# Optimization experiments

Measured on AMD Instinct MI355X. Metric: run time of the kernel, lower is better.

The kernel has to match this reference:

```python
import jax, jax.numpy as jnp
import numpy as np

N = 50000      # nodes
E = 800000     # edges (before self loops)
F_IN = 128
HID = 32
HEADS = 4
OUT_DIM = 1
NEG_SLOPE = 0.2


def gat_conv(x, edge_src, edge_dst, W, a_src, a_dst, bias):
    """PyG GATConv (concat=True, self-loops already appended to edge lists).
    x: [N, Fin], W: [Fin, H*D], a_src/a_dst: [H, D], bias: [H*D]."""
    H, D = a_src.shape
    h = (x @ W).reshape(N, H, D)                      # [N, H, D]
    alpha_src = jnp.einsum('nhd,hd->nh', h, a_src)    # [N, H]
    alpha_dst = jnp.einsum('nhd,hd->nh', h, a_dst)    # [N, H]
    e = alpha_src[edge_src] + alpha_dst[edge_dst]     # [Et, H]
    e = jnp.where(e > 0, e, NEG_SLOPE * e)            # leaky_relu(0.2)
    # softmax over edges grouped by destination node
    m = jax.ops.segment_max(e, edge_dst, num_segments=N)  # [N, H]
    e = jnp.exp(e - jax.lax.stop_gradient(m)[edge_dst])
    s = jax.ops.segment_sum(e, edge_dst, num_segments=N)  # [N, H]
    alpha = e / (s[edge_dst] + 1e-16)                 # [Et, H]
    msg = h[edge_src] * alpha[:, :, None]             # [Et, H, D]
    out = jax.ops.segment_sum(msg, edge_dst, num_segments=N)  # [N, H, D]
    return out.reshape(N, H * D) + bias


def setup_inputs() -> dict:
    key = jax.random.key(0)
    ks = jax.random.split(key, 16)
    HD = HEADS * HID
    def glorot(k, shape, fan_in):
        return jax.random.normal(k, shape, dtype=jnp.float32) / np.sqrt(fan_in)
    inp = {
        'x': jax.random.normal(ks[0], (N, F_IN), dtype=jnp.float32),
        'edge_index': jax.random.randint(ks[1], (2, E), 0, N, dtype=jnp.int64 if jax.config.jax_enable_x64 else jnp.int32),
        'W1': glorot(ks[2], (F_IN, HD), F_IN),
        'a_src1': glorot(ks[3], (HEADS, HID), HID),
        'a_dst1': glorot(ks[4], (HEADS, HID), HID),
        'b1': jnp.zeros((HD,), dtype=jnp.float32),
        'W2': glorot(ks[5], (HD, HD), HD),
        'a_src2': glorot(ks[6], (HEADS, HID), HID),
        'a_dst2': glorot(ks[7], (HEADS, HID), HID),
        'b2': jnp.zeros((HD,), dtype=jnp.float32),
        'Wc1': glorot(ks[8], (HD, HID), HD),
        'bc1': jnp.zeros((HID,), dtype=jnp.float32),
        'Wc2': glorot(ks[9], (HID, OUT_DIM), HID),
        'bc2': jnp.zeros((OUT_DIM,), dtype=jnp.float32),
    }
    return inp


def reference(x, edge_index, W1, a_src1, a_dst1, b1, W2, a_src2, a_dst2, b2,
              Wc1, bc1, Wc2, bc2):
    # PyG add_self_loops=True: append (i -> i) for every node
    loops = jnp.arange(N, dtype=edge_index.dtype)
    src = jnp.concatenate([edge_index[0], loops])
    dst = jnp.concatenate([edge_index[1], loops])
    h = gat_conv(x, src, dst, W1, a_src1, a_dst1, b1)
    h = jax.nn.relu(h)
    h = gat_conv(h, src, dst, W2, a_src2, a_dst2, b2)
    h = jax.nn.relu(h)
    # classifier (dropout is identity at eval)
    h = h @ Wc1 + bc1
    h = h @ Wc2 + bc2
    return jax.nn.sigmoid(h)
```

## Files before the change

kernel.cpp:

```cpp
#include <hip/hip_runtime.h>
#include <hip/hip_bf16.h>
#include <math.h>

#define NEG_SLOPE 0.2f

__device__ __forceinline__ unsigned short f2bf(float f) {
    unsigned int u = __float_as_uint(f);
    u = (u + 0x7fffu + ((u >> 16) & 1u)) >> 16;
    return (unsigned short)u;
}
__device__ __forceinline__ float bflo(unsigned int p) {
    return __uint_as_float(p << 16);
}
__device__ __forceinline__ float bfhi(unsigned int p) {
    return __uint_as_float(p & 0xffff0000u);
}

__device__ __forceinline__ void gemm_alpha_body(
    float* __restrict__ xt,
    const float* __restrict__ X, const float* __restrict__ W,
    const float* __restrict__ a_src, const float* __restrict__ a_dst,
    unsigned short* __restrict__ Hb, float* __restrict__ as_out,
    float* __restrict__ ad_out, int N, int n0, int t)
{
    {
        const float4* src = (const float4*)(X + (size_t)n0 * 128);
        float4* dst = (float4*)xt;
        int rows = N - n0; if (rows > 32) rows = 32;
        int maxv = rows * 32;
        #pragma unroll
        for (int i = 0; i < 4; ++i) {
            int idx = t + i * 256;
            int g = idx < maxv ? idx : maxv - 1;
            dst[idx] = src[g];
        }
    }
    __syncthreads();

    int rg = t >> 5;
    int c  = t & 31;
    int j0 = c * 4;

    float a00=0.f,a01=0.f,a02=0.f,a03=0.f;
    float a10=0.f,a11=0.f,a12=0.f,a13=0.f;
    float a20=0.f,a21=0.f,a22=0.f,a23=0.f;
    float a30=0.f,a31=0.f,a32=0.f,a33=0.f;

    #pragma unroll 4
    for (int k = 0; k < 128; ++k) {
        float4 w = *(const float4*)(W + k * 128 + j0);
        float x0 = xt[(rg     ) * 128 + k];
        float x1 = xt[(rg +  8) * 128 + k];
        float x2 = xt[(rg + 16) * 128 + k];
        float x3 = xt[(rg + 24) * 128 + k];
        a00 = fmaf(x0, w.x, a00); a01 = fmaf(x0, w.y, a01);
        a02 = fmaf(x0, w.z, a02); a03 = fmaf(x0, w.w, a03);
        a10 = fmaf(x1, w.x, a10); a11 = fmaf(x1, w.y, a11);
        a12 = fmaf(x1, w.z, a12); a13 = fmaf(x1, w.w, a13);
        a20 = fmaf(x2, w.x, a20); a21 = fmaf(x2, w.y, a21);
        a22 = fmaf(x2, w.z, a22); a23 = fmaf(x2, w.w, a23);
        a30 = fmaf(x3, w.x, a30); a31 = fmaf(x3, w.y, a31);
        a32 = fmaf(x3, w.z, a32); a33 = fmaf(x3, w.w, a33);
    }

    float4 asv = *(const float4*)(a_src + j0);
    float4 adv = *(const float4*)(a_dst + j0);
    int head = c >> 3;
    int wlane = (c & 7) == 0;

    #pragma unroll
    for (int rr = 0; rr < 4; ++rr) {
        float b0, b1, b2, b3;
        if (rr == 0) { b0=a00; b1=a01; b2=a02; b3=a03; }
        else if (rr == 1) { b0=a10; b1=a11; b2=a12; b3=a13; }
        else if (rr == 2) { b0=a20; b1=a21; b2=a22; b3=a23; }
        else { b0=a30; b1=a31; b2=a32; b3=a33; }
        int row = n0 + rg + rr * 8;
        bool valid = row < N;
        if (valid) {
            unsigned int lo = (unsigned int)f2bf(b0) | ((unsigned int)f2bf(b1) << 16);
            unsigned int hi = (unsigned int)f2bf(b2) | ((unsigned int)f2bf(b3) << 16);
            *(uint2*)(Hb + (size_t)row * 128 + j0) = make_uint2(lo, hi);
        }
        float ps = b0*asv.x + b1*asv.y + b2*asv.z + b3*asv.w;
        float pd = b0*adv.x + b1*adv.y + b2*adv.z + b3*adv.w;
        ps += __shfl_xor(ps, 1, 64); pd += __shfl_xor(pd, 1, 64);
        ps += __shfl_xor(ps, 2, 64); pd += __shfl_xor(pd, 2, 64);
        ps += __shfl_xor(ps, 4, 64); pd += __shfl_xor(pd, 4, 64);
        if (wlane && valid) {
            as_out[row * 4 + head] = ps;
            ad_out[row * 4 + head] = pd;
        }
    }
}

__global__ __launch_bounds__(256) void gemm_alpha_kernel(
    const float* __restrict__ X, const float* __restrict__ W,
    const float* __restrict__ a_src, const float* __restrict__ a_dst,
    unsigned short* __restrict__ Hb, float* __restrict__ as_out,
    float* __restrict__ ad_out, int N)
{
    __shared__ float xt[32 * 128];
    gemm_alpha_body(xt, X, W, a_src, a_dst, Hb, as_out, ad_out, N,
                    blockIdx.x * 32, threadIdx.x);
}

__global__ __launch_bounds__(256) void gemm_fill_kernel(
    const float* __restrict__ X, const float* __restrict__ W,
    const float* __restrict__ a_src, const float* __restrict__ a_dst,
    unsigned short* __restrict__ Hb, float* __restrict__ as_out,
    float* __restrict__ ad_out, int N,
    const int* __restrict__ esrc, int E, int Et,
    const int* __restrict__ offs, const int* __restrict__ pos,
    int* __restrict__ csr, int gemmBlocks, int NS)
{
    __shared__ float xt[32 * 128];
    int g  = blockIdx.x >> 3;
    int l8 = blockIdx.x & 7;
    if ((g & 1) == 0) {
        int gb = (g >> 1) * 8 + l8;
        if (gb < gemmBlocks)
            gemm_alpha_body(xt, X, W, a_src, a_dst, Hb, as_out, ad_out, N,
                            gb * 32, threadIdx.x);
    } else {
        int slice = g >> 1;
        if (slice >= NS) return;
        int rlo = (int)(((long long)N * l8) >> 3);
        int rhi = (int)(((long long)N * (l8 + 1)) >> 3);
        int csrLo = offs[rlo];
        int csrHi = (rhi < N) ? offs[rhi] : Et;
        int e0 = (int)((long long)Et * slice / NS);
        int e1 = (int)((long long)Et * (slice + 1) / NS);
        for (int e = e0 + threadIdx.x; e < e1; e += 256) {
            int p = pos[e];
            if (p >= csrLo && p < csrHi) {
                int s = (e < E) ? esrc[e] : (e - E);
                csr[p] = s;
            }
        }
    }
}

__global__ __launch_bounds__(256) void zero_int_kernel(int* __restrict__ p, int n)
{
    int i = blockIdx.x * 256 + threadIdx.x;
    if (i < n) p[i] = 0;
}

__global__ __launch_bounds__(256) void count_rank_kernel(
    const int* __restrict__ edst, int E, int Et,
    int* __restrict__ cnt, int* __restrict__ rank)
{
    int e = blockIdx.x * 256 + threadIdx.x;
    if (e >= Et) return;
    int d = (e < E) ? edst[e] : (e - E);
    rank[e] = atomicAdd(&cnt[d], 1);
}

__global__ __launch_bounds__(256) void pos_kernel(
    const int* __restrict__ edst, int E, int Et,
    const int* __restrict__ offs, int* __restrict__ rank)
{
    int e = blockIdx.x * 256 + threadIdx.x;
    if (e >= Et) return;
    int d = (e < E) ? edst[e] : (e - E);
    rank[e] = offs[d] + rank[e];
}

__global__ __launch_bounds__(256) void scan_block_kernel(
    const int* __restrict__ in, int* __restrict__ out,
    int* __restrict__ bsum, int n)
{
    __shared__ int sh[256];
    int i = blockIdx.x * 256 + threadIdx.x;
    int v = (i < n) ? in[i] : 0;
    sh[threadIdx.x] = v;
    __syncthreads();
    #pragma unroll
    for (int off = 1; off < 256; off <<= 1) {
        int t = 0;
        if (threadIdx.x >= off) t = sh[threadIdx.x - off];
        __syncthreads();
        if (threadIdx.x >= off) sh[threadIdx.x] += t;
        __syncthreads();
    }
    if (i < n) out[i] = sh[threadIdx.x] - v;
    if (threadIdx.x == 255) bsum[blockIdx.x] = sh[255];
}

__global__ __launch_bounds__(256) void scan_add_kernel(
    int* __restrict__ offs, const int* __restrict__ bsum, int n)
{
    int i = blockIdx.x * 256 + threadIdx.x;
    if (i < n) offs[i] += bsum[blockIdx.x];
}

__global__ __launch_bounds__(256) void gat_fused_kernel(
    const unsigned short* __restrict__ Hb, const int* __restrict__ csr,
    const int* __restrict__ offs, const int* __restrict__ cnt,
    const float* __restrict__ as, const float* __restrict__ ad,
    const float* __restrict__ bias, float* __restrict__ out, int N)
{
    __shared__ float wtab[4 * 256];
    __shared__ int   stab[4 * 64];

    int t = threadIdx.x;
    int wv = t >> 6;
    int g  = (t >> 4) & 3;
    int q  = t & 15;
    int d = blockIdx.x * 16 + (t >> 4);
    if (d >= N) return;
    int start = offs[d];
    int deg = cnt[d];
    float4 adv = *(const float4*)(ad + d * 4);
    int h = q >> 2;
    int f0 = q * 8;

    float m0 = -INFINITY, m1 = -INFINITY, m2 = -INFINITY, m3 = -INFINITY;
    float s0 = 0.f, s1 = 0.f, s2 = 0.f, s3 = 0.f;
    float acc0=0.f,acc1=0.f,acc2=0.f,acc3=0.f,acc4=0.f,acc5=0.f,acc6=0.f,acc7=0.f;

    const float* wbase = wtab + wv * 256 + g * 4 + h;
    const int*   sbase = stab + wv * 64 + g * 16;

    for (int c0 = 0; c0 < deg; c0 += 16) {
        int rem = deg - c0;
        int len = rem < 16 ? rem : 16;
        bool valid = q < len;
        int sidx = valid ? csr[start + c0 + q] : 0;
        float4 av = *(const float4*)(as + sidx * 4);
        float e0 = av.x + adv.x; e0 = e0 > 0.f ? e0 : NEG_SLOPE * e0;
        float e1 = av.y + adv.y; e1 = e1 > 0.f ? e1 : NEG_SLOPE * e1;
        float e2 = av.z + adv.z; e2 = e2 > 0.f ? e2 : NEG_SLOPE * e2;
        float e3 = av.w + adv.w; e3 = e3 > 0.f ? e3 : NEG_SLOPE * e3;
        if (!valid) { e0 = e1 = e2 = e3 = -INFINITY; }

        float c0m = e0, c1m = e1, c2m = e2, c3m = e3;
        #pragma unroll
        for (int off = 8; off; off >>= 1) {
            c0m = fmaxf(c0m, __shfl_xor(c0m, off, 64));
            c1m = fmaxf(c1m, __shfl_xor(c1m, off, 64));
            c2m = fmaxf(c2m, __shfl_xor(c2m, off, 64));
            c3m = fmaxf(c3m, __shfl_xor(c3m, off, 64));
        }
        float nm0 = fmaxf(m0, c0m), nm1 = fmaxf(m1, c1m);
        float nm2 = fmaxf(m2, c2m), nm3 = fmaxf(m3, c3m);
        float r0 = __expf(m0 - nm0), r1 = __expf(m1 - nm1);
        float r2 = __expf(m2 - nm2), r3 = __expf(m3 - nm3);
        m0 = nm0; m1 = nm1; m2 = nm2; m3 = nm3;

        float w0 = valid ? __expf(e0 - m0) : 0.f;
        float w1 = valid ? __expf(e1 - m1) : 0.f;
        float w2 = valid ? __expf(e2 - m2) : 0.f;
        float w3 = valid ? __expf(e3 - m3) : 0.f;

        float t0 = w0, t1 = w1, t2 = w2, t3 = w3;
        #pragma unroll
        for (int off = 8; off; off >>= 1) {
            t0 += __shfl_xor(t0, off, 64);
            t1 += __shfl_xor(t1, off, 64);
            t2 += __shfl_xor(t2, off, 64);
            t3 += __shfl_xor(t3, off, 64);
        }
        s0 = s0 * r0 + t0; s1 = s1 * r1 + t1;
        s2 = s2 * r2 + t2; s3 = s3 * r3 + t3;
        float rs = h == 0 ? r0 : (h == 1 ? r1 : (h == 2 ? r2 : r3));
        acc0 *= rs; acc1 *= rs; acc2 *= rs; acc3 *= rs;
        acc4 *= rs; acc5 *= rs; acc6 *= rs; acc7 *= rs;

        ((float4*)wtab)[wv * 64 + q * 4 + g] = make_float4(w0, w1, w2, w3);
        stab[wv * 64 + g * 16 + q] = sidx;

        int kk = 0;
        for (; kk + 4 <= len; kk += 4) {
            int sk0 = sbase[kk+0], sk1 = sbase[kk+1];
            int sk2 = sbase[kk+2], sk3 = sbase[kk+3];
            float wa = wbase[(kk+0)*16], wb = wbase[(kk+1)*16];
            float wc = wbase[(kk+2)*16], wd = wbase[(kk+3)*16];
            uint4 p0 = *(const uint4*)(Hb + (size_t)sk0 * 128 + f0);
            uint4 p1 = *(const uint4*)(Hb + (size_t)sk1 * 128 + f0);
            uint4 p2 = *(const uint4*)(Hb + (size_t)sk2 * 128 + f0);
            uint4 p3 = *(const uint4*)(Hb + (size_t)sk3 * 128 + f0);
            acc0 = fmaf(wa, bflo(p0.x), acc0); acc1 = fmaf(wa, bfhi(p0.x), acc1);
            acc2 = fmaf(wa, bflo(p0.y), acc2); acc3 = fmaf(wa, bfhi(p0.y), acc3);
            acc4 = fmaf(wa, bflo(p0.z), acc4); acc5 = fmaf(wa, bfhi(p0.z), acc5);
            acc6 = fmaf(wa, bflo(p0.w), acc6); acc7 = fmaf(wa, bfhi(p0.w), acc7);
            acc0 = fmaf(wb, bflo(p1.x), acc0); acc1 = fmaf(wb, bfhi(p1.x), acc1);
            acc2 = fmaf(wb, bflo(p1.y), acc2); acc3 = fmaf(wb, bfhi(p1.y), acc3);
            acc4 = fmaf(wb, bflo(p1.z), acc4); acc5 = fmaf(wb, bfhi(p1.z), acc5);
            acc6 = fmaf(wb, bflo(p1.w), acc6); acc7 = fmaf(wb, bfhi(p1.w), acc7);
            acc0 = fmaf(wc, bflo(p2.x), acc0); acc1 = fmaf(wc, bfhi(p2.x), acc1);
            acc2 = fmaf(wc, bflo(p2.y), acc2); acc3 = fmaf(wc, bfhi(p2.y), acc3);
            acc4 = fmaf(wc, bflo(p2.z), acc4); acc5 = fmaf(wc, bfhi(p2.z), acc5);
            acc6 = fmaf(wc, bflo(p2.w), acc6); acc7 = fmaf(wc, bfhi(p2.w), acc7);
            acc0 = fmaf(wd, bflo(p3.x), acc0); acc1 = fmaf(wd, bfhi(p3.x), acc1);
            acc2 = fmaf(wd, bflo(p3.y), acc2); acc3 = fmaf(wd, bfhi(p3.y), acc3);
            acc4 = fmaf(wd, bflo(p3.z), acc4); acc5 = fmaf(wd, bfhi(p3.z), acc5);
            acc6 = fmaf(wd, bflo(p3.w), acc6); acc7 = fmaf(wd, bfhi(p3.w), acc7);
        }
        for (; kk < len; ++kk) {
            int sk = sbase[kk];
            float wk = wbase[kk*16];
            uint4 p = *(const uint4*)(Hb + (size_t)sk * 128 + f0);
            acc0 = fmaf(wk, bflo(p.x), acc0); acc1 = fmaf(wk, bfhi(p.x), acc1);
            acc2 = fmaf(wk, bflo(p.y), acc2); acc3 = fmaf(wk, bfhi(p.y), acc3);
            acc4 = fmaf(wk, bflo(p.z), acc4); acc5 = fmaf(wk, bfhi(p.z), acc5);
            acc6 = fmaf(wk, bflo(p.w), acc6); acc7 = fmaf(wk, bfhi(p.w), acc7);
        }
    }

    float sh = h == 0 ? s0 : (h == 1 ? s1 : (h == 2 ? s2 : s3));
    float inv = 1.f / (sh + 1e-16f);
    float4 bA = *(const float4*)(bias + f0);
    float4 bB = *(const float4*)(bias + f0 + 4);
    float4 oA = make_float4(fmaxf(acc0 * inv + bA.x, 0.f),
                            fmaxf(acc1 * inv + bA.y, 0.f),
                            fmaxf(acc2 * inv + bA.z, 0.f),
                            fmaxf(acc3 * inv + bA.w, 0.f));
    float4 oB = make_float4(fmaxf(acc4 * inv + bB.x, 0.f),
                            fmaxf(acc5 * inv + bB.y, 0.f),
                            fmaxf(acc6 * inv + bB.z, 0.f),
                            fmaxf(acc7 * inv + bB.w, 0.f));
    *(float4*)(out + (size_t)d * 128 + f0)     = oA;
    *(float4*)(out + (size_t)d * 128 + f0 + 4) = oB;
}

__global__ __launch_bounds__(256) void classifier_kernel(
    const float* __restrict__ X, const float* __restrict__ Wc1,
    const float* __restrict__ bc1, const float* __restrict__ Wc2,
    const float* __restrict__ bc2, float* __restrict__ out, int N)
{
    int n = blockIdx.x * 8 + (threadIdx.x >> 5);
    if (n >= N) return;
    int j = threadIdx.x & 31;
    const float* xrow = X + (size_t)n * 128;
    float acc = bc1[j];
    #pragma unroll 8
    for (int k = 0; k < 128; ++k)
        acc = fmaf(xrow[k], Wc1[k * 32 + j], acc);
    float y = acc * Wc2[j];
    #pragma unroll
    for (int off = 16; off; off >>= 1) y += __shfl_xor(y, off, 64);
    if (j == 0)
        out[n] = 1.0f / (1.0f + expf(-(y + bc2[0])));
}

extern "C" void kernel_launch(void* const* d_in, const int* in_sizes, int n_in,
                              void* d_out, int out_size, void* d_ws, size_t ws_size,
                              hipStream_t stream)
{
    const float* x      = (const float*)d_in[0];
    const int*   eidx   = (const int*)d_in[1];
    const float* W1     = (const float*)d_in[2];
    const float* a_src1 = (const float*)d_in[3];
    const float* a_dst1 = (const float*)d_in[4];
    const float* b1     = (const float*)d_in[5];
    const float* W2     = (const float*)d_in[6];
    const float* a_src2 = (const float*)d_in[7];
    const float* a_dst2 = (const float*)d_in[8];
    const float* b2     = (const float*)d_in[9];
    const float* Wc1    = (const float*)d_in[10];
    const float* bc1    = (const float*)d_in[11];
    const float* Wc2    = (const float*)d_in[12];
    const float* bc2    = (const float*)d_in[13];

    int N  = in_sizes[0] / 128;
    int E  = in_sizes[1] / 2;
    int Et = E + N;
    const int* esrc = eidx;
    const int* edst = eidx + E;

    char* wsb = (char*)d_ws;
    unsigned short* Hb = (unsigned short*)wsb;  wsb += (size_t)N * 128 * 2;
    float*  f1_buf = (float*)wsb;   wsb += (size_t)N * 128 * 4;
    float*  as_buf = (float*)wsb;   wsb += (size_t)N * 4 * 4;
    float*  ad_buf = (float*)wsb;   wsb += (size_t)N * 4 * 4;
    int*    cnt    = (int*)wsb;     wsb += (size_t)N * 4;
    int*    offs   = (int*)wsb;     wsb += (size_t)N * 4;
    int*    bsum   = (int*)wsb;     wsb += 512 * 4;
    int*    csr    = (int*)wsb;     wsb += (size_t)Et * 4;
    int*    rank   = (int*)wsb;     wsb += (size_t)Et * 4;

    int nbN = (N + 255) / 256;
    int nbE = (Et + 255) / 256;
    int gemmBlocks = (N + 31) / 32;
    int gemmGroups = (gemmBlocks + 7) / 8;
    int NS = gemmGroups;
    int fusedGrid = gemmGroups * 2 * 8;

    zero_int_kernel<<<nbN, 256, 0, stream>>>(cnt, N);
    count_rank_kernel<<<nbE, 256, 0, stream>>>(edst, E, Et, cnt, rank);
    scan_block_kernel<<<nbN, 256, 0, stream>>>(cnt, offs, bsum, N);
    scan_block_kernel<<<1, 256, 0, stream>>>(bsum, bsum, &bsum[300], nbN);
    scan_add_kernel<<<nbN, 256, 0, stream>>>(offs, bsum, N);
    pos_kernel<<<nbE, 256, 0, stream>>>(edst, E, Et, offs, rank);

    gemm_fill_kernel<<<fusedGrid, 256, 0, stream>>>(
        x, W1, a_src1, a_dst1, Hb, as_buf, ad_buf, N,
        esrc, E, Et, offs, rank, csr, gemmBlocks, NS);
    gat_fused_kernel<<<(N + 15) / 16, 256, 0, stream>>>(Hb, csr, offs, cnt,
                                                        as_buf, ad_buf, b1, f1_buf, N);
    gemm_alpha_kernel<<<gemmBlocks, 256, 0, stream>>>(f1_buf, W2, a_src2, a_dst2,
                                                      Hb, as_buf, ad_buf, N);
    gat_fused_kernel<<<(N + 15) / 16, 256, 0, stream>>>(Hb, csr, offs, cnt,
                                                        as_buf, ad_buf, b2, f1_buf, N);

    classifier_kernel<<<(N + 7) / 8, 256, 0, stream>>>(f1_buf, Wc1, bc1, Wc2, bc2,
                                                       (float*)d_out, N);
}
```

Measured before the change: 368.5 us.

## Fold classifier into second GAT layer, split fill from GEMM, enlarge GEMM tile

```diff
diff --git a/kernel.cpp b/kernel.cpp
--- a/kernel.cpp
+++ b/kernel.cpp
@@ -16,20 +16,23 @@
     return __uint_as_float(p & 0xffff0000u);
 }
 
-__device__ __forceinline__ void gemm_alpha_body(
-    float* __restrict__ xt,
+__global__ __launch_bounds__(256) void gemm_alpha_kernel(
     const float* __restrict__ X, const float* __restrict__ W,
     const float* __restrict__ a_src, const float* __restrict__ a_dst,
     unsigned short* __restrict__ Hb, float* __restrict__ as_out,
-    float* __restrict__ ad_out, int N, int n0, int t)
-{
+    float* __restrict__ ad_out, int N)
+{
+    __shared__ float xt[64 * 128];
+    int n0 = blockIdx.x * 64;
+    int t  = threadIdx.x;
+
     {
         const float4* src = (const float4*)(X + (size_t)n0 * 128);
         float4* dst = (float4*)xt;
-        int rows = N - n0; if (rows > 32) rows = 32;
+        int rows = N - n0; if (rows > 64) rows = 64;
         int maxv = rows * 32;
         #pragma unroll
-        for (int i = 0; i < 4; ++i) {
+        for (int i = 0; i < 8; ++i) {
             int idx = t + i * 256;
             int g = idx < maxv ? idx : maxv - 1;
             dst[idx] = src[g];
@@ -41,26 +44,22 @@
     int c  = t & 31;
     int j0 = c * 4;
 
-    float a00=0.f,a01=0.f,a02=0.f,a03=0.f;
-    float a10=0.f,a11=0.f,a12=0.f,a13=0.f;
-    float a20=0.f,a21=0.f,a22=0.f,a23=0.f;
-    float a30=0.f,a31=0.f,a32=0.f,a33=0.f;
-
-    #pragma unroll 4
+    float acc[8][4];
+    #pragma unroll
+    for (int rr = 0; rr < 8; ++rr)
+        { acc[rr][0]=0.f; acc[rr][1]=0.f; acc[rr][2]=0.f; acc[rr][3]=0.f; }
+
+    #pragma unroll 2
     for (int k = 0; k < 128; ++k) {
         float4 w = *(const float4*)(W + k * 128 + j0);
-        float x0 = xt[(rg     ) * 128 + k];
-        float x1 = xt[(rg +  8) * 128 + k];
-        float x2 = xt[(rg + 16) * 128 + k];
-        float x3 = xt[(rg + 24) * 128 + k];
-        a00 = fmaf(x0, w.x, a00); a01 = fmaf(x0, w.y, a01);
-        a02 = fmaf(x0, w.z, a02); a03 = fmaf(x0, w.w, a03);
-        a10 = fmaf(x1, w.x, a10); a11 = fmaf(x1, w.y, a11);
-        a12 = fmaf(x1, w.z, a12); a13 = fmaf(x1, w.w, a13);
-        a20 = fmaf(x2, w.x, a20); a21 = fmaf(x2, w.y, a21);
-        a22 = fmaf(x2, w.z, a22); a23 = fmaf(x2, w.w, a23);
-        a30 = fmaf(x3, w.x, a30); a31 = fmaf(x3, w.y, a31);
-        a32 = fmaf(x3, w.z, a32); a33 = fmaf(x3, w.w, a33);
+        #pragma unroll
+        for (int rr = 0; rr < 8; ++rr) {
+            float xv = xt[(rg + rr * 8) * 128 + k];
+            acc[rr][0] = fmaf(xv, w.x, acc[rr][0]);
+            acc[rr][1] = fmaf(xv, w.y, acc[rr][1]);
+            acc[rr][2] = fmaf(xv, w.z, acc[rr][2]);
+            acc[rr][3] = fmaf(xv, w.w, acc[rr][3]);
+        }
     }
 
     float4 asv = *(const float4*)(a_src + j0);
@@ -69,12 +68,8 @@
     int wlane = (c & 7) == 0;
 
     #pragma unroll
-    for (int rr = 0; rr < 4; ++rr) {
-        float b0, b1, b2, b3;
-        if (rr == 0) { b0=a00; b1=a01; b2=a02; b3=a03; }
-        else if (rr == 1) { b0=a10; b1=a11; b2=a12; b3=a13; }
-        else if (rr == 2) { b0=a20; b1=a21; b2=a22; b3=a23; }
-        else { b0=a30; b1=a31; b2=a32; b3=a33; }
+    for (int rr = 0; rr < 8; ++rr) {
+        float b0 = acc[rr][0], b1 = acc[rr][1], b2 = acc[rr][2], b3 = acc[rr][3];
         int row = n0 + rg + rr * 8;
         bool valid = row < N;
         if (valid) {
@@ -90,53 +85,6 @@
         if (wlane && valid) {
             as_out[row * 4 + head] = ps;
             ad_out[row * 4 + head] = pd;
-        }
-    }
-}
-
-__global__ __launch_bounds__(256) void gemm_alpha_kernel(
-    const float* __restrict__ X, const float* __restrict__ W,
-    const float* __restrict__ a_src, const float* __restrict__ a_dst,
-    unsigned short* __restrict__ Hb, float* __restrict__ as_out,
-    float* __restrict__ ad_out, int N)
-{
-    __shared__ float xt[32 * 128];
-    gemm_alpha_body(xt, X, W, a_src, a_dst, Hb, as_out, ad_out, N,
-                    blockIdx.x * 32, threadIdx.x);
-}
-
-__global__ __launch_bounds__(256) void gemm_fill_kernel(
-    const float* __restrict__ X, const float* __restrict__ W,
-    const float* __restrict__ a_src, const float* __restrict__ a_dst,
-    unsigned short* __restrict__ Hb, float* __restrict__ as_out,
-    float* __restrict__ ad_out, int N,
-    const int* __restrict__ esrc, int E, int Et,
-    const int* __restrict__ offs, const int* __restrict__ pos,
-    int* __restrict__ csr, int gemmBlocks, int NS)
-{
-    __shared__ float xt[32 * 128];
-    int g  = blockIdx.x >> 3;
-    int l8 = blockIdx.x & 7;
-    if ((g & 1) == 0) {
-        int gb = (g >> 1) * 8 + l8;
-        if (gb < gemmBlocks)
-            gemm_alpha_body(xt, X, W, a_src, a_dst, Hb, as_out, ad_out, N,
-                            gb * 32, threadIdx.x);
-    } else {
-        int slice = g >> 1;
-        if (slice >= NS) return;
-        int rlo = (int)(((long long)N * l8) >> 3);
-        int rhi = (int)(((long long)N * (l8 + 1)) >> 3);
-        int csrLo = offs[rlo];
-        int csrHi = (rhi < N) ? offs[rhi] : Et;
-        int e0 = (int)((long long)Et * slice / NS);
-        int e1 = (int)((long long)Et * (slice + 1) / NS);
-        for (int e = e0 + threadIdx.x; e < e1; e += 256) {
-            int p = pos[e];
-            if (p >= csrLo && p < csrHi) {
-                int s = (e < E) ? esrc[e] : (e - E);
-                csr[p] = s;
-            }
         }
     }
 }
@@ -195,11 +143,52 @@
     if (i < n) offs[i] += bsum[blockIdx.x];
 }
 
+__global__ __launch_bounds__(256) void fill_kernel(
+    const int* __restrict__ esrc, int E, int Et, int N,
+    const int* __restrict__ offs, const int* __restrict__ pos,
+    int* __restrict__ csr, int S)
+{
+    int slice = blockIdx.x >> 3;
+    int l8 = blockIdx.x & 7;
+    if (slice >= S) return;
+    int rlo = (int)(((long long)N * l8) >> 3);
+    int rhi = (int)(((long long)N * (l8 + 1)) >> 3);
+    int csrLo = offs[rlo];
+    int csrHi = (rhi < N) ? offs[rhi] : Et;
+    int e0 = (int)((long long)Et * slice / S);
+    int e1 = (int)((long long)Et * (slice + 1) / S);
+    for (int e = e0 + threadIdx.x; e < e1; e += 256) {
+        int p = pos[e];
+        if (p >= csrLo && p < csrHi)
+            csr[p] = (e < E) ? esrc[e] : (e - E);
+    }
+}
+
+__global__ __launch_bounds__(128) void cls_vec_kernel(
+    const float* __restrict__ Wc1, const float* __restrict__ bc1,
+    const float* __restrict__ Wc2, const float* __restrict__ bc2,
+    float* __restrict__ v)
+{
+    int i = threadIdx.x;
+    float acc = 0.f;
+    #pragma unroll
+    for (int j = 0; j < 32; ++j)
+        acc = fmaf(Wc1[i * 32 + j], Wc2[j], acc);
+    v[i] = acc;
+    if (i == 0) {
+        float c = bc2[0];
+        for (int j = 0; j < 32; ++j)
+            c = fmaf(bc1[j], Wc2[j], c);
+        v[128] = c;
+    }
+}
+
 __global__ __launch_bounds__(256) void gat_fused_kernel(
     const unsigned short* __restrict__ Hb, const int* __restrict__ csr,
     const int* __restrict__ offs, const int* __restrict__ cnt,
     const float* __restrict__ as, const float* __restrict__ ad,
-    const float* __restrict__ bias, float* __restrict__ out, int N)
+    const float* __restrict__ bias, float* __restrict__ out, int N,
+    const float* __restrict__ v, float* __restrict__ dcls, int docls)
 {
     __shared__ float wtab[4 * 256];
     __shared__ int   stab[4 * 64];
@@ -313,36 +302,30 @@
     float inv = 1.f / (sh + 1e-16f);
     float4 bA = *(const float4*)(bias + f0);
     float4 bB = *(const float4*)(bias + f0 + 4);
-    float4 oA = make_float4(fmaxf(acc0 * inv + bA.x, 0.f),
-                            fmaxf(acc1 * inv + bA.y, 0.f),
-                            fmaxf(acc2 * inv + bA.z, 0.f),
-                            fmaxf(acc3 * inv + bA.w, 0.f));
-    float4 oB = make_float4(fmaxf(acc4 * inv + bB.x, 0.f),
-                            fmaxf(acc5 * inv + bB.y, 0.f),
-                            fmaxf(acc6 * inv + bB.z, 0.f),
-                            fmaxf(acc7 * inv + bB.w, 0.f));
-    *(float4*)(out + (size_t)d * 128 + f0)     = oA;
-    *(float4*)(out + (size_t)d * 128 + f0 + 4) = oB;
-}
-
-__global__ __launch_bounds__(256) void classifier_kernel(
-    const float* __restrict__ X, const float* __restrict__ Wc1,
-    const float* __restrict__ bc1, const float* __restrict__ Wc2,
-    const float* __restrict__ bc2, float* __restrict__ out, int N)
-{
-    int n = blockIdx.x * 8 + (threadIdx.x >> 5);
-    if (n >= N) return;
-    int j = threadIdx.x & 31;
-    const float* xrow = X + (size_t)n * 128;
-    float acc = bc1[j];
-    #pragma unroll 8
-    for (int k = 0; k < 128; ++k)
-        acc = fmaf(xrow[k], Wc1[k * 32 + j], acc);
-    float y = acc * Wc2[j];
-    #pragma unroll
-    for (int off = 16; off; off >>= 1) y += __shfl_xor(y, off, 64);
-    if (j == 0)
-        out[n] = 1.0f / (1.0f + expf(-(y + bc2[0])));
+    float o0 = fmaxf(acc0 * inv + bA.x, 0.f);
+    float o1 = fmaxf(acc1 * inv + bA.y, 0.f);
+    float o2 = fmaxf(acc2 * inv + bA.z, 0.f);
+    float o3 = fmaxf(acc3 * inv + bA.w, 0.f);
+    float o4 = fmaxf(acc4 * inv + bB.x, 0.f);
+    float o5 = fmaxf(acc5 * inv + bB.y, 0.f);
+    float o6 = fmaxf(acc6 * inv + bB.z, 0.f);
+    float o7 = fmaxf(acc7 * inv + bB.w, 0.f);
+
+    if (!docls) {
+        *(float4*)(out + (size_t)d * 128 + f0)     = make_float4(o0, o1, o2, o3);
+        *(float4*)(out + (size_t)d * 128 + f0 + 4) = make_float4(o4, o5, o6, o7);
+    } else {
+        float4 vA = *(const float4*)(v + f0);
+        float4 vB = *(const float4*)(v + f0 + 4);
+        float part = o0*vA.x + o1*vA.y + o2*vA.z + o3*vA.w
+                   + o4*vB.x + o5*vB.y + o6*vB.z + o7*vB.w;
+        part += __shfl_xor(part, 1, 64);
+        part += __shfl_xor(part, 2, 64);
+        part += __shfl_xor(part, 4, 64);
+        part += __shfl_xor(part, 8, 64);
+        if (q == 0)
+            dcls[d] = 1.0f / (1.0f + __expf(-(part + v[128])));
+    }
 }
 
 extern "C" void kernel_launch(void* const* d_in, const int* in_sizes, int n_in,
@@ -380,13 +363,12 @@
     int*    bsum   = (int*)wsb;     wsb += 512 * 4;
     int*    csr    = (int*)wsb;     wsb += (size_t)Et * 4;
     int*    rank   = (int*)wsb;     wsb += (size_t)Et * 4;
+    float*  vcls   = (float*)wsb;   wsb += 132 * 4;
 
     int nbN = (N + 255) / 256;
     int nbE = (Et + 255) / 256;
-    int gemmBlocks = (N + 31) / 32;
-    int gemmGroups = (gemmBlocks + 7) / 8;
-    int NS = gemmGroups;
-    int fusedGrid = gemmGroups * 2 * 8;
+    int gemmBlocks = (N + 63) / 64;
+    int S = 512;
 
     zero_int_kernel<<<nbN, 256, 0, stream>>>(cnt, N);
     count_rank_kernel<<<nbE, 256, 0, stream>>>(edst, E, Et, cnt, rank);
@@ -394,17 +376,15 @@
     scan_block_kernel<<<1, 256, 0, stream>>>(bsum, bsum, &bsum[300], nbN);
     scan_add_kernel<<<nbN, 256, 0, stream>>>(offs, bsum, N);
     pos_kernel<<<nbE, 256, 0, stream>>>(edst, E, Et, offs, rank);
-
-    gemm_fill_kernel<<<fusedGrid, 256, 0, stream>>>(
-        x, W1, a_src1, a_dst1, Hb, as_buf, ad_buf, N,
-        esrc, E, Et, offs, rank, csr, gemmBlocks, NS);
+    cls_vec_kernel<<<1, 128, 0, stream>>>(Wc1, bc1, Wc2, bc2, vcls);
+    fill_kernel<<<S * 8, 256, 0, stream>>>(esrc, E, Et, N, offs, rank, csr, S);
+
+    gemm_alpha_kernel<<<gemmBlocks, 256, 0, stream>>>(x, W1, a_src1, a_dst1,
+                                                      Hb, as_buf, ad_buf, N);
     gat_fused_kernel<<<(N + 15) / 16, 256, 0, stream>>>(Hb, csr, offs, cnt,
-                                                        as_buf, ad_buf, b1, f1_buf, N);
+        as_buf, ad_buf, b1, f1_buf, N, vcls, (float*)d_out, 0);
     gemm_alpha_kernel<<<gemmBlocks, 256, 0, stream>>>(f1_buf, W2, a_src2, a_dst2,
                                                       Hb, as_buf, ad_buf, N);
     gat_fused_kernel<<<(N + 15) / 16, 256, 0, stream>>>(Hb, csr, offs, cnt,
-                                                        as_buf, ad_buf, b2, f1_buf, N);
-
-    classifier_kernel<<<(N + 7) / 8, 256, 0, stream>>>(f1_buf, Wc1, bc1, Wc2, bc2,
-                                                       (float*)d_out, N);
-}
+        as_buf, ad_buf, b2, f1_buf, N, vcls, (float*)d_out, 1);
+}
```

Measured after the change: 310.7 us. 1.19x faster.
